# Kernel tuning notes

Hardware: AMD Instinct MI355X
Metric: run time of the kernel (lower is better)

Reference implementation:

```python
import jax, jax.numpy as jnp
import numpy as np

B, N, D = 4, 4096, 1024
LN_EPS = 1e-5

def setup_inputs() -> dict:
    key = jax.random.key(0)
    ks = jax.random.split(key, 12)
    s = 1.0 / np.sqrt(D)
    return {
        "embeddings": jax.random.normal(ks[0], (B, N, D), dtype=jnp.float32),
        "edge_indices": jax.random.randint(ks[1], (2, 8192), 0, N, dtype=jnp.int64),
        "edge_times": jax.random.uniform(ks[2], (8192,), dtype=jnp.float32),
        "timestamps": jax.random.uniform(ks[3], (N,), dtype=jnp.float32),
        "Wq": jax.random.uniform(ks[4], (D, D), jnp.float32, -s, s),
        "bq": jax.random.uniform(ks[5], (D,), jnp.float32, -s, s),
        "Wk": jax.random.uniform(ks[6], (D, D), jnp.float32, -s, s),
        "bk": jax.random.uniform(ks[7], (D,), jnp.float32, -s, s),
        "Wv": jax.random.uniform(ks[8], (D, D), jnp.float32, -s, s),
        "bv": jax.random.uniform(ks[9], (D,), jnp.float32, -s, s),
        "gamma": jnp.ones((D,), jnp.float32),
        "beta": jnp.zeros((D,), jnp.float32),
    }

def reference(embeddings, edge_indices, edge_times, timestamps,
              Wq, bq, Wk, bk, Wv, bv, gamma, beta):
    # edge_indices / edge_times / timestamps are unused by the original forward.
    d = embeddings.shape[-1]
    q = jnp.einsum("bnd,ed->bne", embeddings, Wq) + bq   # [B,N,D]
    k = jnp.einsum("bnd,ed->bne", embeddings, Wk) + bk
    v = jnp.einsum("bnd,ed->bne", embeddings, Wv) + bv
    scores = jnp.einsum("bnd,bmd->bnm", q, k) / jnp.sqrt(jnp.asarray(d, embeddings.dtype))
    attn = jax.nn.softmax(scores, axis=-1)                # [B,N,N]
    attended = jnp.einsum("bnm,bmd->bnd", attn, v)
    x = embeddings + attended
    mu = jnp.mean(x, axis=-1, keepdims=True)
    var = jnp.mean(jnp.square(x - mu), axis=-1, keepdims=True)
    return gamma * (x - mu) * jax.lax.rsqrt(var + LN_EPS) + beta
```

## Files before the change

### kernel.cpp

```cpp
#include <hip/hip_runtime.h>
#include <hip/hip_fp8.h>

typedef unsigned short u16;
typedef unsigned char  u8;
typedef long long      i64;
using bf16x8 = __attribute__((ext_vector_type(8))) __bf16;
using f32x4  = __attribute__((ext_vector_type(4))) float;

__device__ __forceinline__ u16 f2bf(float f) {
    unsigned u = __builtin_bit_cast(unsigned, f);
    u += 0x7fffu + ((u >> 16) & 1u);
    return (u16)(u >> 16);
}
__device__ __forceinline__ float bf2f(u16 h) {
    unsigned u = ((unsigned)h) << 16;
    return __builtin_bit_cast(float, u);
}
__device__ __forceinline__ u8 f2fp8(float f) {
    __hip_fp8_e4m3 t(f);
    return t.__x;
}
__device__ __forceinline__ float wred_sum(float v) {
    #pragma unroll
    for (int o = 32; o; o >>= 1) v += __shfl_xor(v, o, 64);
    return v;
}

__device__ __forceinline__ void gl2lds16(const void* g, void* l) {
    __builtin_amdgcn_global_load_lds(
        (__attribute__((address_space(1))) void*)(g),
        (__attribute__((address_space(3))) void*)(l), 16, 0, 0);
}

__global__ __launch_bounds__(256)
void cast_bf16(const float* __restrict__ src, u16* __restrict__ dst, int n4) {
    int i = blockIdx.x * 256 + threadIdx.x;
    if (i < n4) {
        float4 f = ((const float4*)src)[i];
        ushort4 u;
        u.x = f2bf(f.x); u.y = f2bf(f.y); u.z = f2bf(f.z); u.w = f2bf(f.w);
        ((ushort4*)dst)[i] = u;
    }
}

__global__ __launch_bounds__(256)
void cast_v_fp8(const u16* __restrict__ src, u8* __restrict__ dst, int n8) {
    int i = blockIdx.x * 256 + threadIdx.x;
    if (i < n8) {
        ushort4 a = ((const ushort4*)src)[2 * i];
        ushort4 b = ((const ushort4*)src)[2 * i + 1];
        union { u8 c[8]; unsigned long long q; } r;
        r.c[0] = f2fp8(bf2f(a.x)); r.c[1] = f2fp8(bf2f(a.y));
        r.c[2] = f2fp8(bf2f(a.z)); r.c[3] = f2fp8(bf2f(a.w));
        r.c[4] = f2fp8(bf2f(b.x)); r.c[5] = f2fp8(bf2f(b.y));
        r.c[6] = f2fp8(bf2f(b.z)); r.c[7] = f2fp8(bf2f(b.w));
        ((unsigned long long*)dst)[i] = r.q;
    }
}

template<int MODE, int TM, bool SWAP>
__global__ __launch_bounds__(256, 4)
void gemm_bt(const u16* __restrict__ A, const u16* __restrict__ Bt, const int K,
             u16* __restrict__ oQ, u16* __restrict__ oK, u16* __restrict__ oVt,
             const float* __restrict__ bQ, const float* __restrict__ bK,
             const float* __restrict__ bV,
             u8* __restrict__ oP, float* __restrict__ sums, const float scale)
{
    __shared__ u16 smem[TM * 32 + 128 * 32];
    u16* As = smem;
    u16* Bs = smem + TM * 32;

    constexpr int IM = TM / 32;
    const int tid  = threadIdx.x;
    const int wv   = tid >> 6;
    const int lane = tid & 63;
    const int wr   = (wv >> 1) * (TM / 2);
    const int wc   = (wv & 1) << 6;

    const int row0 = (SWAP ? blockIdx.x : blockIdx.y) * TM;
    const int col0 = (SWAP ? blockIdx.y : blockIdx.x) * 128;

    const int srow = tid >> 2;
    const int scol = (((tid & 3) ^ ((tid >> 3) & 3)) << 3);

    const u16* pA0 = A  + (size_t)(row0 + srow) * K + scol;
    const u16* pB0 = Bt + (size_t)(col0 + srow) * K + scol;

    char* aB0 = (char*)As + wv * 1024;
    char* aB1 = (char*)As + 4096 + wv * 1024;
    char* bB0 = (char*)Bs + wv * 1024;
    char* bB1 = (char*)Bs + 4096 + wv * 1024;

    const int fr = lane & 15;
    const int g  = lane >> 4;
    const int sw = (fr >> 1) & 3;
    const int kc = ((g ^ sw) << 3);

    f32x4 acc[IM][4];
    #pragma unroll
    for (int i = 0; i < IM; i++)
        #pragma unroll
        for (int j = 0; j < 4; j++) acc[i][j] = (f32x4){0.f, 0.f, 0.f, 0.f};

    for (int k0 = 0; k0 < K; k0 += 32) {
        __syncthreads();
        gl2lds16(pA0 + k0, aB0);
        if (TM == 128) gl2lds16(pA0 + (size_t)64 * K + k0, aB1);
        gl2lds16(pB0 + k0, bB0);
        gl2lds16(pB0 + (size_t)64 * K + k0, bB1);
        __syncthreads();

        bf16x8 af[IM], bfr[4];
        #pragma unroll
        for (int i = 0; i < IM; i++) af[i]  = *(const bf16x8*)&As[(wr + 16 * i + fr) * 32 + kc];
        #pragma unroll
        for (int j = 0; j < 4; j++)  bfr[j] = *(const bf16x8*)&Bs[(wc + 16 * j + fr) * 32 + kc];
        #pragma unroll
        for (int i = 0; i < IM; i++)
            #pragma unroll
            for (int j = 0; j < 4; j++)
                acc[i][j] = __builtin_amdgcn_mfma_f32_16x16x32_bf16(af[i], bfr[j], acc[i][j], 0, 0, 0);
    }

    const int rB = (lane >> 4) << 2;
    const int cB = lane & 15;

    if (MODE == 0) {
        const int sel = col0 >> 10;
        if (sel < 2) {
            const float* bias = (sel == 0) ? bQ : bK;
            u16* dst = (sel == 0) ? oQ : oK;
            #pragma unroll
            for (int i = 0; i < IM; i++) {
                #pragma unroll
                for (int j = 0; j < 4; j++) {
                    const int m0 = row0 + wr + 16 * i + rB;
                    const int e  = (col0 & 1023) + wc + 16 * j + cB;
                    const float bb = bias[e];
                    #pragma unroll
                    for (int t = 0; t < 4; t++)
                        dst[(size_t)(m0 + t) * 1024 + e] = f2bf(acc[i][j][t] + bb);
                }
            }
        } else {
            const int b      = row0 >> 12;
            const int n_base = row0 & 4095;
            const int e0     = col0 & 1023;
            __syncthreads();
            #pragma unroll
            for (int P = 0; P < 2; ++P) {
                if ((wc >> 6) == P) {
                    #pragma unroll
                    for (int i = 0; i < IM; i++) {
                        const int n_l0 = wr + 16 * i + rB;
                        const int hq   = n_l0 >> 3;
                        const int off  = n_l0 & 7;
                        #pragma unroll
                        for (int j = 0; j < 4; j++) {
                            const int e_p = 16 * j + cB;
                            const int hp  = hq ^ (e_p & 7);
                            const float bb = bV[e0 + P * 64 + e_p];
                            ushort4 pk;
                            pk.x = f2bf(acc[i][j][0] + bb);
                            pk.y = f2bf(acc[i][j][1] + bb);
                            pk.z = f2bf(acc[i][j][2] + bb);
                            pk.w = f2bf(acc[i][j][3] + bb);
                            *(ushort4*)&smem[e_p * 128 + hp * 8 + off] = pk;
                        }
                    }
                }
                __syncthreads();
                #pragma unroll
                for (int p4 = 0; p4 < 4; ++p4) {
                    const int idx = p4 * 256 + tid;
                    const int er  = idx >> 4;
                    const int c   = idx & 15;
                    const int cc  = c ^ (er & 7);
                    int4 v = *(const int4*)&smem[er * 128 + cc * 8];
                    *(int4*)&oVt[(size_t)b * 4194304 +
                                 (size_t)(e0 + P * 64 + er) * 4096 + n_base + c * 8] = v;
                }
                if (P == 0) __syncthreads();
            }
        }
    } else {
        float psum[IM][4];
        #pragma unroll
        for (int i = 0; i < IM; i++)
            #pragma unroll
            for (int t = 0; t < 4; t++) psum[i][t] = 0.f;

        #pragma unroll
        for (int i = 0; i < IM; i++) {
            #pragma unroll
            for (int j = 0; j < 4; j++) {
                const int m0 = row0 + wr + 16 * i + rB;
                const int c  = col0 + wc + 16 * j + cB;
                #pragma unroll
                for (int t = 0; t < 4; t++) {
                    const float e = __expf(acc[i][j][t] * scale);
                    psum[i][t] += e;
                    oP[(size_t)(m0 + t) * 4096 + c] = f2fp8(e);
                }
            }
        }
        #pragma unroll
        for (int i = 0; i < IM; i++) {
            #pragma unroll
            for (int t = 0; t < 4; t++) {
                float v = psum[i][t];
                v += __shfl_xor(v, 1, 64);
                v += __shfl_xor(v, 2, 64);
                v += __shfl_xor(v, 4, 64);
                v += __shfl_xor(v, 8, 64);
                if (cB == 0)
                    atomicAdd(&sums[row0 + wr + 16 * i + rB + t], v);
            }
        }
    }
}

__global__ __launch_bounds__(256, 4)
void pv_fp8(const u8* __restrict__ p0, const u8* __restrict__ p1,
            const u8* __restrict__ p2, const u8* __restrict__ p3,
            const u8* __restrict__ vt8, const float* __restrict__ sums,
            float* __restrict__ out)
{
    __shared__ u8 As[128 * 64];
    __shared__ u8 Bs[128 * 64];

    const int b = blockIdx.z;
    const u8* Pb = (b == 0) ? p0 : (b == 1) ? p1 : (b == 2) ? p2 : p3;
    const u8* Vb = vt8 + (size_t)b * 4194304;
    const float* sm = sums + (b << 12);
    float* Ob = out + (size_t)b * 4194304;

    const int tid = threadIdx.x, wv = tid >> 6, lane = tid & 63;
    const int wr = (wv >> 1) << 6, wc = (wv & 1) << 6;
    const int row0 = blockIdx.x << 7, col0 = blockIdx.y << 7;

    const int sc8 = (((tid & 3) ^ ((tid >> 3) & 3)) << 4);
    const u8* gA0 = Pb + (size_t)(row0 + (tid >> 2)) * 4096 + sc8;
    const u8* gA1 = gA0 + (size_t)64 * 4096;
    const u8* gB0 = Vb + (size_t)(col0 + (tid >> 2)) * 4096 + sc8;
    const u8* gB1 = gB0 + (size_t)64 * 4096;
    char* aL0 = (char*)As + wv * 1024;
    char* aL1 = (char*)As + 4096 + wv * 1024;
    char* bL0 = (char*)Bs + wv * 1024;
    char* bL1 = (char*)Bs + 4096 + wv * 1024;

    const int fr = lane & 15;
    const int g  = lane >> 4;
    const int sw = (fr >> 1) & 3;
    const int h8 = (g & 1) << 3;
    const int g2 = g >> 1;

    f32x4 acc[4][4];
    #pragma unroll
    for (int i = 0; i < 4; i++)
        #pragma unroll
        for (int j = 0; j < 4; j++) acc[i][j] = (f32x4){0.f, 0.f, 0.f, 0.f};

    for (int n0 = 0; n0 < 4096; n0 += 64) {
        __syncthreads();
        gl2lds16(gA0 + n0, aL0);
        gl2lds16(gA1 + n0, aL1);
        gl2lds16(gB0 + n0, bL0);
        gl2lds16(gB1 + n0, bL1);
        __syncthreads();
        #pragma unroll
        for (int kk = 0; kk < 64; kk += 32) {
            const int pc = (((kk >> 4) + g2) ^ sw) << 4;
            i64 af[4], bf[4];
            #pragma unroll
            for (int i = 0; i < 4; i++) af[i] = *(const i64*)&As[(wr + 16 * i + fr) * 64 + pc + h8];
            #pragma unroll
            for (int j = 0; j < 4; j++) bf[j] = *(const i64*)&Bs[(wc + 16 * j + fr) * 64 + pc + h8];
            #pragma unroll
            for (int i = 0; i < 4; i++)
                #pragma unroll
                for (int j = 0; j < 4; j++)
                    acc[i][j] = __builtin_amdgcn_mfma_f32_16x16x32_fp8_fp8(af[i], bf[j], acc[i][j], 0, 0, 0);
        }
    }

    const int rB = (lane >> 4) << 2, cB = lane & 15;
    #pragma unroll
    for (int i = 0; i < 4; i++) {
        const int m0 = row0 + wr + 16 * i + rB;
        const float i0 = 1.0f / sm[m0];
        const float i1 = 1.0f / sm[m0 + 1];
        const float i2 = 1.0f / sm[m0 + 2];
        const float i3 = 1.0f / sm[m0 + 3];
        #pragma unroll
        for (int j = 0; j < 4; j++) {
            const int e = col0 + wc + 16 * j + cB;
            Ob[(size_t)(m0 + 0) * 1024 + e] = acc[i][j][0] * i0;
            Ob[(size_t)(m0 + 1) * 1024 + e] = acc[i][j][1] * i1;
            Ob[(size_t)(m0 + 2) * 1024 + e] = acc[i][j][2] * i2;
            Ob[(size_t)(m0 + 3) * 1024 + e] = acc[i][j][3] * i3;
        }
    }
}

__global__ __launch_bounds__(256)
void residual_ln(const float* __restrict__ emb, float* __restrict__ out,
                 const float* __restrict__ gamma, const float* __restrict__ beta) {
    const size_t row = blockIdx.x;
    const int t = threadIdx.x;
    const int wv = t >> 6, lane = t & 63;
    const size_t base = row * 1024 + t * 4;

    float4 ev = *(const float4*)(emb + base);
    float4 ov = *(const float4*)(out + base);
    float x0 = ev.x + ov.x, x1 = ev.y + ov.y, x2 = ev.z + ov.z, x3 = ev.w + ov.w;

    float s = x0 + x1 + x2 + x3;
    float q = x0 * x0 + x1 * x1 + x2 * x2 + x3 * x3;
    s = wred_sum(s);
    q = wred_sum(q);
    __shared__ float s1[4], s2[4];
    if (lane == 0) { s1[wv] = s; s2[wv] = q; }
    __syncthreads();
    s = s1[0] + s1[1] + s1[2] + s1[3];
    q = s2[0] + s2[1] + s2[2] + s2[3];

    const float mu  = s * (1.0f / 1024.0f);
    const float var = q * (1.0f / 1024.0f) - mu * mu;
    const float r   = rsqrtf(var + 1e-5f);

    float4 g  = *(const float4*)(gamma + t * 4);
    float4 be = *(const float4*)(beta + t * 4);
    float4 res;
    res.x = (x0 - mu) * r * g.x + be.x;
    res.y = (x1 - mu) * r * g.y + be.y;
    res.z = (x2 - mu) * r * g.z + be.z;
    res.w = (x3 - mu) * r * g.w + be.w;
    *(float4*)(out + base) = res;
}

extern "C" void kernel_launch(void* const* d_in, const int* in_sizes, int n_in,
                              void* d_out, int out_size, void* d_ws, size_t ws_size,
                              hipStream_t stream) {
    const float* emb   = (const float*)d_in[0];
    const float* Wq    = (const float*)d_in[4];
    const float* bq    = (const float*)d_in[5];
    const float* Wk    = (const float*)d_in[6];
    const float* bk    = (const float*)d_in[7];
    const float* Wv    = (const float*)d_in[8];
    const float* bv    = (const float*)d_in[9];
    const float* gamma = (const float*)d_in[10];
    const float* beta  = (const float*)d_in[11];
    float* out = (float*)d_out;

    char* ws = (char*)d_ws;
    if (ws_size < 140509184u) return;
    u16* Xbf = (u16*)(ws);
    u16* Wbf = (u16*)(ws + 33554432);
    u16* Qbf = (u16*)(ws + 39845888);
    u16* Kbf = (u16*)(ws + 73400320);
    u16* VTB = (u16*)(ws + 106954752);

    u8*    VT8  = (u8*)(ws);
    u8*    P0   = (u8*)(ws + 16777216);
    float* SUMS = (float*)(ws + 33554432);
    u8*    P1   = (u8*)(ws + 106954752);
    u8*    P2   = (u8*)(ws + 123731968);
    u8*    P3   = (u8*)(ws + 39845888);
    u8*    Pb[4] = {P0, P1, P2, P3};

    cast_bf16<<<16384, 256, 0, stream>>>(emb, Xbf, 4194304);
    cast_bf16<<<1024, 256, 0, stream>>>(Wq, Wbf,           262144);
    cast_bf16<<<1024, 256, 0, stream>>>(Wk, Wbf + 1048576, 262144);
    cast_bf16<<<1024, 256, 0, stream>>>(Wv, Wbf + 2097152, 262144);

    gemm_bt<0, 128, true><<<dim3(128, 24), 256, 0, stream>>>(Xbf, Wbf, 1024,
        Qbf, Kbf, VTB, bq, bk, bv, nullptr, nullptr, 1.0f);

    cast_v_fp8<<<8192, 256, 0, stream>>>(VTB, VT8, 2097152);

    hipMemsetAsync(SUMS, 0, 65536, stream);

    for (int b = 0; b < 4; ++b) {
        const size_t o = (size_t)b * 4194304;
        gemm_bt<1, 128, false><<<dim3(32, 32), 256, 0, stream>>>(Qbf + o, Kbf + o, 1024,
            nullptr, nullptr, nullptr, nullptr, nullptr, nullptr,
            Pb[b], SUMS + b * 4096, 0.03125f);
    }

    pv_fp8<<<dim3(32, 8, 4), 256, 0, stream>>>(P0, P1, P2, P3, VT8, SUMS, out);

    residual_ln<<<16384, 256, 0, stream>>>(emb, out, gamma, beta);
}
```

Measured before the change: 590.9 us.

## Replace QK and PV GEMMs with 256x256-tile, 8-wave, 4-stage pipelined kernels

The QK^T score GEMM and the fp8 PV GEMM get new dedicated kernels. Each uses 512 threads, 256x256 output tiles, and a 4-slot LDS ring fed by async global-to-LDS loads, with split barriers and setprio around the MFMA blocks. The aim is to hide global load latency and raise arithmetic intensity compared with the earlier single-stage 128x128 loops. In exchange, the kernels use far more LDS and registers, which lowers occupancy, and the grids become much smaller (256 blocks per batch for QK, 256 blocks total for PV), so there is a risk of wave-quantization and underutilizing the CUs.

```diff
diff --git a/kernel.cpp b/kernel.cpp
--- a/kernel.cpp
+++ b/kernel.cpp
@@ -183,118 +183,226 @@
                 if (P == 0) __syncthreads();
             }
         }
-    } else {
-        float psum[IM][4];
-        #pragma unroll
-        for (int i = 0; i < IM; i++)
-            #pragma unroll
-            for (int t = 0; t < 4; t++) psum[i][t] = 0.f;
-
-        #pragma unroll
-        for (int i = 0; i < IM; i++) {
-            #pragma unroll
-            for (int j = 0; j < 4; j++) {
-                const int m0 = row0 + wr + 16 * i + rB;
-                const int c  = col0 + wc + 16 * j + cB;
-                #pragma unroll
-                for (int t = 0; t < 4; t++) {
-                    const float e = __expf(acc[i][j][t] * scale);
-                    psum[i][t] += e;
-                    oP[(size_t)(m0 + t) * 4096 + c] = f2fp8(e);
-                }
+    }
+}
+
+__global__ __launch_bounds__(512, 2)
+void gemm_s8(const u16* __restrict__ Q, const u16* __restrict__ Km,
+             u8* __restrict__ P, float* __restrict__ sm, const float scale)
+{
+    __shared__ u16 smem[65536];
+    const int tid = threadIdx.x;
+    const int wv = tid >> 6, lane = tid & 63;
+    const int wm = wv >> 2, wn = wv & 3;
+    const int row0 = blockIdx.x << 8, col0 = blockIdx.y << 8;
+
+    const int srow = tid >> 2;
+    const int scol = ((tid & 3) ^ ((tid >> 3) & 3)) << 3;
+    const u16* gA = Q  + (size_t)(row0 + srow) * 1024 + scol;
+    const u16* gB = Km + (size_t)(col0 + srow) * 1024 + scol;
+    char* lds = (char*)smem;
+    const int wvo = wv << 10;
+
+    const int fr = lane & 15, g = lane >> 4;
+    const int kc = (g ^ ((fr >> 1) & 3)) << 4;
+
+    f32x4 acc[8][4];
+    #pragma unroll
+    for (int i = 0; i < 8; i++)
+        #pragma unroll
+        for (int j = 0; j < 4; j++) acc[i][j] = (f32x4){0.f, 0.f, 0.f, 0.f};
+
+    #define SG_A(ts, sl) { \
+        gl2lds16(gA + (ts) * 32,          lds + (sl) * 32768 + wvo); \
+        gl2lds16(gA + 131072 + (ts) * 32, lds + (sl) * 32768 + 8192 + wvo); }
+    #define SG_B(ts, sl) { \
+        gl2lds16(gB + (ts) * 32,          lds + (sl) * 32768 + 16384 + wvo); \
+        gl2lds16(gB + 131072 + (ts) * 32, lds + (sl) * 32768 + 24576 + wvo); }
+
+    SG_A(0, 0); SG_B(0, 0);
+    SG_A(1, 1); SG_B(1, 1);
+    SG_A(2, 2); SG_B(2, 2);
+
+    for (int t = 0; t < 32; ++t) {
+        const int slot = t & 3;
+        const int ts = (t + 3) & 31;
+        const int ns = (t + 3) & 3;
+        const char* Ab = lds + slot * 32768;
+        const char* Bb = Ab + 16384;
+
+        asm volatile("s_waitcnt vmcnt(8)" ::: "memory");
+        __builtin_amdgcn_s_barrier();
+        __builtin_amdgcn_sched_barrier(0);
+
+        SG_A(ts, ns);
+        bf16x8 bf[4], af[4];
+        #pragma unroll
+        for (int j = 0; j < 4; ++j)
+            bf[j] = *(const bf16x8*)(Bb + (wn * 64 + 16 * j + fr) * 64 + kc);
+        #pragma unroll
+        for (int i = 0; i < 4; ++i)
+            af[i] = *(const bf16x8*)(Ab + (wm * 128 + 16 * i + fr) * 64 + kc);
+        __builtin_amdgcn_s_setprio(1);
+        #pragma unroll
+        for (int i = 0; i < 4; ++i)
+            #pragma unroll
+            for (int j = 0; j < 4; ++j)
+                acc[i][j] = __builtin_amdgcn_mfma_f32_16x16x32_bf16(af[i], bf[j], acc[i][j], 0, 0, 0);
+        __builtin_amdgcn_s_setprio(0);
+        __builtin_amdgcn_s_barrier();
+
+        SG_B(ts, ns);
+        #pragma unroll
+        for (int i = 0; i < 4; ++i)
+            af[i] = *(const bf16x8*)(Ab + (wm * 128 + 64 + 16 * i + fr) * 64 + kc);
+        __builtin_amdgcn_s_setprio(1);
+        #pragma unroll
+        for (int i = 0; i < 4; ++i)
+            #pragma unroll
+            for (int j = 0; j < 4; ++j)
+                acc[i + 4][j] = __builtin_amdgcn_mfma_f32_16x16x32_bf16(af[i], bf[j], acc[i + 4][j], 0, 0, 0);
+        __builtin_amdgcn_s_setprio(0);
+    }
+    #undef SG_A
+    #undef SG_B
+
+    const int rB = (lane >> 4) << 2, cB = lane & 15;
+    float psum[8][4];
+    #pragma unroll
+    for (int i = 0; i < 8; i++)
+        #pragma unroll
+        for (int t = 0; t < 4; t++) psum[i][t] = 0.f;
+
+    #pragma unroll
+    for (int i = 0; i < 8; i++) {
+        const int m0 = row0 + wm * 128 + 16 * i + rB;
+        #pragma unroll
+        for (int j = 0; j < 4; j++) {
+            const int c = col0 + wn * 64 + 16 * j + cB;
+            #pragma unroll
+            for (int t = 0; t < 4; t++) {
+                const float e = __expf(acc[i][j][t] * scale);
+                psum[i][t] += e;
+                P[(size_t)(m0 + t) * 4096 + c] = f2fp8(e);
             }
         }
-        #pragma unroll
-        for (int i = 0; i < IM; i++) {
-            #pragma unroll
-            for (int t = 0; t < 4; t++) {
-                float v = psum[i][t];
-                v += __shfl_xor(v, 1, 64);
-                v += __shfl_xor(v, 2, 64);
-                v += __shfl_xor(v, 4, 64);
-                v += __shfl_xor(v, 8, 64);
-                if (cB == 0)
-                    atomicAdd(&sums[row0 + wr + 16 * i + rB + t], v);
-            }
+    }
+    #pragma unroll
+    for (int i = 0; i < 8; i++) {
+        #pragma unroll
+        for (int t = 0; t < 4; t++) {
+            float v = psum[i][t];
+            v += __shfl_xor(v, 1, 64);
+            v += __shfl_xor(v, 2, 64);
+            v += __shfl_xor(v, 4, 64);
+            v += __shfl_xor(v, 8, 64);
+            if (cB == 0)
+                atomicAdd(&sm[row0 + wm * 128 + 16 * i + rB + t], v);
         }
     }
 }
 
-__global__ __launch_bounds__(256, 4)
-void pv_fp8(const u8* __restrict__ p0, const u8* __restrict__ p1,
-            const u8* __restrict__ p2, const u8* __restrict__ p3,
-            const u8* __restrict__ vt8, const float* __restrict__ sums,
-            float* __restrict__ out)
+__global__ __launch_bounds__(512, 2)
+void pv8(const u8* __restrict__ p0, const u8* __restrict__ p1,
+         const u8* __restrict__ p2, const u8* __restrict__ p3,
+         const u8* __restrict__ vt8, const float* __restrict__ sums,
+         float* __restrict__ out)
 {
-    __shared__ u8 As[128 * 64];
-    __shared__ u8 Bs[128 * 64];
-
+    __shared__ u8 smem[131072];
     const int b = blockIdx.z;
     const u8* Pb = (b == 0) ? p0 : (b == 1) ? p1 : (b == 2) ? p2 : p3;
     const u8* Vb = vt8 + (size_t)b * 4194304;
     const float* sm = sums + (b << 12);
     float* Ob = out + (size_t)b * 4194304;
 
-    const int tid = threadIdx.x, wv = tid >> 6, lane = tid & 63;
-    const int wr = (wv >> 1) << 6, wc = (wv & 1) << 6;
-    const int row0 = blockIdx.x << 7, col0 = blockIdx.y << 7;
-
-    const int sc8 = (((tid & 3) ^ ((tid >> 3) & 3)) << 4);
-    const u8* gA0 = Pb + (size_t)(row0 + (tid >> 2)) * 4096 + sc8;
-    const u8* gA1 = gA0 + (size_t)64 * 4096;
-    const u8* gB0 = Vb + (size_t)(col0 + (tid >> 2)) * 4096 + sc8;
-    const u8* gB1 = gB0 + (size_t)64 * 4096;
-    char* aL0 = (char*)As + wv * 1024;
-    char* aL1 = (char*)As + 4096 + wv * 1024;
-    char* bL0 = (char*)Bs + wv * 1024;
-    char* bL1 = (char*)Bs + 4096 + wv * 1024;
-
-    const int fr = lane & 15;
-    const int g  = lane >> 4;
+    const int tid = threadIdx.x;
+    const int wv = tid >> 6, lane = tid & 63;
+    const int wm = wv >> 2, wn = wv & 3;
+    const int row0 = blockIdx.x << 8, col0 = blockIdx.y << 8;
+
+    const int srow = tid >> 2;
+    const int sc16 = ((tid & 3) ^ ((tid >> 3) & 3)) << 4;
+    const u8* gA = Pb + (size_t)(row0 + srow) * 4096 + sc16;
+    const u8* gB = Vb + (size_t)(col0 + srow) * 4096 + sc16;
+    char* lds = (char*)smem;
+    const int wvo = wv << 10;
+
+    const int fr = lane & 15, g = lane >> 4;
     const int sw = (fr >> 1) & 3;
-    const int h8 = (g & 1) << 3;
-    const int g2 = g >> 1;
-
-    f32x4 acc[4][4];
-    #pragma unroll
-    for (int i = 0; i < 4; i++)
+    const int g2 = g >> 1, h8 = (g & 1) << 3;
+    const int pc0 = ((g2 ^ sw) << 4) + h8;
+    const int pc1 = (((2 + g2) ^ sw) << 4) + h8;
+
+    f32x4 acc[8][4];
+    #pragma unroll
+    for (int i = 0; i < 8; i++)
         #pragma unroll
         for (int j = 0; j < 4; j++) acc[i][j] = (f32x4){0.f, 0.f, 0.f, 0.f};
 
-    for (int n0 = 0; n0 < 4096; n0 += 64) {
-        __syncthreads();
-        gl2lds16(gA0 + n0, aL0);
-        gl2lds16(gA1 + n0, aL1);
-        gl2lds16(gB0 + n0, bL0);
-        gl2lds16(gB1 + n0, bL1);
-        __syncthreads();
-        #pragma unroll
-        for (int kk = 0; kk < 64; kk += 32) {
-            const int pc = (((kk >> 4) + g2) ^ sw) << 4;
-            i64 af[4], bf[4];
-            #pragma unroll
-            for (int i = 0; i < 4; i++) af[i] = *(const i64*)&As[(wr + 16 * i + fr) * 64 + pc + h8];
-            #pragma unroll
-            for (int j = 0; j < 4; j++) bf[j] = *(const i64*)&Bs[(wc + 16 * j + fr) * 64 + pc + h8];
-            #pragma unroll
-            for (int i = 0; i < 4; i++)
-                #pragma unroll
-                for (int j = 0; j < 4; j++)
-                    acc[i][j] = __builtin_amdgcn_mfma_f32_16x16x32_fp8_fp8(af[i], bf[j], acc[i][j], 0, 0, 0);
-        }
-    }
+    #define PG_A(ts, sl) { \
+        gl2lds16(gA + (ts) * 64,          lds + (sl) * 32768 + wvo); \
+        gl2lds16(gA + 524288 + (ts) * 64, lds + (sl) * 32768 + 8192 + wvo); }
+    #define PG_B(ts, sl) { \
+        gl2lds16(gB + (ts) * 64,          lds + (sl) * 32768 + 16384 + wvo); \
+        gl2lds16(gB + 524288 + (ts) * 64, lds + (sl) * 32768 + 24576 + wvo); }
+
+    PG_A(0, 0); PG_B(0, 0);
+    PG_A(1, 1); PG_B(1, 1);
+    PG_A(2, 2); PG_B(2, 2);
+
+    for (int t = 0; t < 64; ++t) {
+        const int slot = t & 3;
+        const int ts = (t + 3) & 63;
+        const int ns = (t + 3) & 3;
+        const char* Ab = lds + slot * 32768;
+        const char* Bb = Ab + 16384;
+
+        asm volatile("s_waitcnt vmcnt(8)" ::: "memory");
+        __builtin_amdgcn_s_barrier();
+        __builtin_amdgcn_sched_barrier(0);
+
+        PG_A(ts, ns);
+        i64 af[8], bf[4];
+        #pragma unroll
+        for (int i = 0; i < 8; ++i) af[i] = *(const i64*)(Ab + (wm * 128 + 16 * i + fr) * 64 + pc0);
+        #pragma unroll
+        for (int j = 0; j < 4; ++j) bf[j] = *(const i64*)(Bb + (wn * 64 + 16 * j + fr) * 64 + pc0);
+        __builtin_amdgcn_s_setprio(1);
+        #pragma unroll
+        for (int i = 0; i < 8; ++i)
+            #pragma unroll
+            for (int j = 0; j < 4; ++j)
+                acc[i][j] = __builtin_amdgcn_mfma_f32_16x16x32_fp8_fp8(af[i], bf[j], acc[i][j], 0, 0, 0);
+        __builtin_amdgcn_s_setprio(0);
+        __builtin_amdgcn_s_barrier();
+
+        PG_B(ts, ns);
+        #pragma unroll
+        for (int i = 0; i < 8; ++i) af[i] = *(const i64*)(Ab + (wm * 128 + 16 * i + fr) * 64 + pc1);
+        #pragma unroll
+        for (int j = 0; j < 4; ++j) bf[j] = *(const i64*)(Bb + (wn * 64 + 16 * j + fr) * 64 + pc1);
+        __builtin_amdgcn_s_setprio(1);
+        #pragma unroll
+        for (int i = 0; i < 8; ++i)
+            #pragma unroll
+            for (int j = 0; j < 4; ++j)
+                acc[i][j] = __builtin_amdgcn_mfma_f32_16x16x32_fp8_fp8(af[i], bf[j], acc[i][j], 0, 0, 0);
+        __builtin_amdgcn_s_setprio(0);
+    }
+    #undef PG_A
+    #undef PG_B
 
     const int rB = (lane >> 4) << 2, cB = lane & 15;
     #pragma unroll
-    for (int i = 0; i < 4; i++) {
-        const int m0 = row0 + wr + 16 * i + rB;
+    for (int i = 0; i < 8; i++) {
+        const int m0 = row0 + wm * 128 + 16 * i + rB;
         const float i0 = 1.0f / sm[m0];
         const float i1 = 1.0f / sm[m0 + 1];
         const float i2 = 1.0f / sm[m0 + 2];
         const float i3 = 1.0f / sm[m0 + 3];
         #pragma unroll
         for (int j = 0; j < 4; j++) {
-            const int e = col0 + wc + 16 * j + cB;
+            const int e = col0 + wn * 64 + 16 * j + cB;
             Ob[(size_t)(m0 + 0) * 1024 + e] = acc[i][j][0] * i0;
             Ob[(size_t)(m0 + 1) * 1024 + e] = acc[i][j][1] * i1;
             Ob[(size_t)(m0 + 2) * 1024 + e] = acc[i][j][2] * i2;
@@ -383,12 +491,11 @@
 
     for (int b = 0; b < 4; ++b) {
         const size_t o = (size_t)b * 4194304;
-        gemm_bt<1, 128, false><<<dim3(32, 32), 256, 0, stream>>>(Qbf + o, Kbf + o, 1024,
-            nullptr, nullptr, nullptr, nullptr, nullptr, nullptr,
+        gemm_s8<<<dim3(16, 16), 512, 0, stream>>>(Qbf + o, Kbf + o,
             Pb[b], SUMS + b * 4096, 0.03125f);
     }
 
-    pv_fp8<<<dim3(32, 8, 4), 256, 0, stream>>>(P0, P1, P2, P3, VT8, SUMS, out);
+    pv8<<<dim3(16, 4, 4), 512, 0, stream>>>(P0, P1, P2, P3, VT8, SUMS, out);
 
     residual_ln<<<16384, 256, 0, stream>>>(emb, out, gamma, beta);
 }
```

Measured after the change: 602.0 us. No clear change (+1.9%).
